# Optimization experiments

Measured on AMD Instinct MI355X. Metric: run time of the kernel, lower is better.

Reference implementation:

```python
import math
import jax, jax.numpy as jnp
import numpy as np

B, S, HID = 2, 2048, 3072
NH, HD = 32, 96            # num_heads, head_dim; num_kv_heads == num_heads (n_rep = 1)
OP = NH * HD + 2 * (NH * HD)  # 9216


def _rope_tables(seq_len, head_dim, theta=10000.0):
    inv_freq = 1.0 / (theta ** (np.arange(0, head_dim, 2, dtype=np.float32) / head_dim))
    t = np.arange(seq_len, dtype=np.float32)
    freqs = np.outer(t, inv_freq)                      # [S, HD/2]
    emb = np.concatenate([freqs, freqs], axis=-1)      # [S, HD]
    return jnp.asarray(np.cos(emb)), jnp.asarray(np.sin(emb))


def setup_inputs() -> dict:
    key = jax.random.key(0)
    k1, k2, k3 = jax.random.split(key, 3)
    hidden_states = jax.random.normal(k1, (B, S, HID), dtype=jnp.float32)
    cos, sin = _rope_tables(S, HD)
    # additive causal mask [B, 1, S, S]
    neg = jnp.finfo(jnp.float32).min
    causal = jnp.where(jnp.tril(jnp.ones((S, S), dtype=bool)), 0.0, neg)
    attention_mask = jnp.broadcast_to(causal[None, None], (B, 1, S, S)).astype(jnp.float32)
    Wqkv = jax.random.normal(k2, (HID, OP), dtype=jnp.float32) * (HID ** -0.5)
    Wo = jax.random.normal(k3, (NH * HD, HID), dtype=jnp.float32) * ((NH * HD) ** -0.5)
    return {"hidden_states": hidden_states, "cos": cos, "sin": sin,
            "attention_mask": attention_mask, "Wqkv": Wqkv, "Wo": Wo}


def _rotate_half(x):
    x1, x2 = jnp.split(x, 2, axis=-1)
    return jnp.concatenate([-x2, x1], axis=-1)


def reference(hidden_states, cos, sin, attention_mask, Wqkv, Wo):
    bsz, q_len, _ = hidden_states.shape
    qkv = hidden_states @ Wqkv                                    # [B,S,OP]
    q, k, v = jnp.split(qkv, [NH * HD, 2 * NH * HD], axis=-1)
    # [B,S,H*D] -> [B,H,S,D]
    to_bhsd = lambda t: t.reshape(bsz, q_len, NH, HD).transpose(0, 2, 1, 3)
    q, k, v = to_bhsd(q), to_bhsd(k), to_bhsd(v)
    c = cos[None, None]                                           # [1,1,S,D]
    s = sin[None, None]
    q = q * c + _rotate_half(q) * s
    k = k * c + _rotate_half(k) * s
    # num_key_value_groups == 1, so repeat_kv is identity.
    scores = jnp.einsum('bhqd,bhkd->bhqk', q, k) / math.sqrt(HD)  # [B,H,S,S]
    scores = scores + attention_mask
    attn = jax.nn.softmax(scores.astype(jnp.float32), axis=-1).astype(v.dtype)
    # dropout p=0.0 / eval -> identity
    out = jnp.einsum('bhqk,bhkd->bhqd', attn, v)                  # [B,H,S,D]
    out = out.transpose(0, 2, 1, 3).reshape(bsz, q_len, NH * HD)
    return out @ Wo                                               # [B,S,HID]
```

## Files before the change

kernel.cpp:

```cpp
#include <hip/hip_runtime.h>

typedef __bf16  bf16x8 __attribute__((ext_vector_type(8)));
typedef float   f32x4  __attribute__((ext_vector_type(4)));
typedef float   f32x16 __attribute__((ext_vector_type(16)));
typedef short   i16x8  __attribute__((ext_vector_type(8)));
typedef unsigned short u16x4 __attribute__((ext_vector_type(4)));
typedef unsigned int   u32x4 __attribute__((ext_vector_type(4)));

__device__ __forceinline__ float bf2f(unsigned short u) {
    union { unsigned int i; float f; } v; v.i = ((unsigned int)u) << 16; return v.f;
}
__device__ __forceinline__ unsigned short f2bf(float f) {
    union { float f; unsigned int i; } v; v.f = f;
    unsigned int r = v.i + 0x7FFFu + ((v.i >> 16) & 1u);
    return (unsigned short)(r >> 16);
}
__device__ __forceinline__ unsigned packbf(float lo, float hi) {
    return (unsigned)f2bf(lo) | ((unsigned)f2bf(hi) << 16);
}
__device__ __forceinline__ void gload_lds16(const void* g, void* l) {
    __builtin_amdgcn_global_load_lds(
        (const __attribute__((address_space(1))) void*)g,
        (__attribute__((address_space(3))) void*)l, 16, 0, 0);
}
__device__ __forceinline__ void pswap(unsigned &x, unsigned &y) {
#if __has_builtin(__builtin_amdgcn_permlane32_swap)
    auto r = __builtin_amdgcn_permlane32_swap((int)x, (int)y, false, false);
    x = (unsigned)r[0]; y = (unsigned)r[1];
#else
    unsigned nx = (threadIdx.x & 32) ? (unsigned)__shfl_xor((int)y, 32) : x;
    unsigned ny = (threadIdx.x & 32) ? y : (unsigned)__shfl_xor((int)x, 32);
    x = nx; y = ny;
#endif
}
__device__ __forceinline__ float partner_f(float v, int hi) {
    unsigned x = __builtin_bit_cast(unsigned, v), y = x;
    pswap(x, y);
    return __builtin_bit_cast(float, hi ? x : y);
}

__global__ __launch_bounds__(256) void cast_f32_bf16(
    const float* __restrict__ in, unsigned short* __restrict__ out, int n8)
{
    int i = blockIdx.x * 256 + threadIdx.x;
    if (i >= n8) return;
    const f32x4* p = (const f32x4*)(in + (long)i * 8);
    f32x4 a = p[0], b = p[1];
    i16x8 o;
    o[0]=(short)f2bf(a[0]); o[1]=(short)f2bf(a[1]); o[2]=(short)f2bf(a[2]); o[3]=(short)f2bf(a[3]);
    o[4]=(short)f2bf(b[0]); o[5]=(short)f2bf(b[1]); o[6]=(short)f2bf(b[2]); o[7]=(short)f2bf(b[3]);
    *(i16x8*)(out + (long)i * 8) = o;
}

__global__ __launch_bounds__(256) void transpose_cast(
    const float* __restrict__ in, unsigned short* __restrict__ out, int R, int C)
{
    __shared__ float tile[64][65];
    int c0 = blockIdx.x * 64, r0 = blockIdx.y * 64;
    int tx = threadIdx.x & 63, ty = threadIdx.x >> 6;
#pragma unroll
    for (int i = 0; i < 64; i += 4)
        tile[ty + i][tx] = in[(long)(r0 + ty + i) * C + c0 + tx];
    __syncthreads();
#pragma unroll
    for (int i = 0; i < 64; i += 4)
        out[(long)(c0 + ty + i) * R + r0 + tx] = f2bf(tile[tx][ty + i]);
}

template <int MODE>
__global__ __launch_bounds__(256) void gemm_bt(
    const unsigned short* __restrict__ A, const unsigned short* __restrict__ B,
    int K, int N,
    unsigned short* __restrict__ Qo, unsigned short* __restrict__ Ko,
    unsigned short* __restrict__ Vo, float* __restrict__ Cf)
{
    __shared__ unsigned short Al[128 * 64];
    __shared__ unsigned short Bl[128 * 64];
    const int t = threadIdx.x;
    const int w = t >> 6, l = t & 63, lhi = l >> 4, llo = l & 15;
    const int m0 = blockIdx.x * 128, n0 = blockIdx.y * 128;
    const int wmo = (w >> 1) << 6, wno = (w & 1) << 6;

    const unsigned short* ag[4];
    const unsigned short* bg[4];
#pragma unroll
    for (int i = 0; i < 4; ++i) {
        int j = i * 256 + t;
        int row = j >> 3;
        int c = (j & 7) ^ (row & 7);
        ag[i] = A + (long)(m0 + row) * K + c * 8;
        bg[i] = B + (long)(n0 + row) * K + c * 8;
    }

    f32x4 acc[4][4] = {};
    const int nkt = K >> 6;
    for (int kt = 0; kt < nkt; ++kt) {
        __syncthreads();
#pragma unroll
        for (int i = 0; i < 4; ++i) {
            gload_lds16(ag[i] + kt * 64, &Al[(i * 256 + (w << 6)) * 8]);
            gload_lds16(bg[i] + kt * 64, &Bl[(i * 256 + (w << 6)) * 8]);
        }
        __syncthreads();
#pragma unroll
        for (int kf = 0; kf < 2; ++kf) {
            bf16x8 af[4], bfv[4];
#pragma unroll
            for (int mi = 0; mi < 4; ++mi) {
                int row = wmo + mi * 16 + llo;
                int cc = (kf * 4 + lhi) ^ (row & 7);
                af[mi] = __builtin_bit_cast(bf16x8, *(const i16x8*)&Al[row * 64 + cc * 8]);
            }
#pragma unroll
            for (int ni = 0; ni < 4; ++ni) {
                int row = wno + ni * 16 + llo;
                int cc = (kf * 4 + lhi) ^ (row & 7);
                bfv[ni] = __builtin_bit_cast(bf16x8, *(const i16x8*)&Bl[row * 64 + cc * 8]);
            }
#pragma unroll
            for (int mi = 0; mi < 4; ++mi)
#pragma unroll
                for (int ni = 0; ni < 4; ++ni)
                    acc[mi][ni] = __builtin_amdgcn_mfma_f32_16x16x32_bf16(
                        af[mi], bfv[ni], acc[mi][ni], 0, 0, 0);
        }
    }

#pragma unroll
    for (int mi = 0; mi < 4; ++mi) {
        int s0g = m0 + wmo + mi * 16 + (lhi << 2);
#pragma unroll
        for (int ni = 0; ni < 4; ++ni) {
            int gcol = n0 + wno + ni * 16 + llo;
            if (MODE == 1) {
#pragma unroll
                for (int r = 0; r < 4; ++r)
                    Cf[(long)(s0g + r) * N + gcol] = acc[mi][ni][r];
            } else {
                int seg = gcol / 3072;
                int cc2 = gcol - seg * 3072;
                int h = cc2 / 96, d = cc2 - h * 96;
                int b = s0g >> 11, s = s0g & 2047;
                long bh = (long)((b << 5) + h);
                if (seg == 2) {
                    u16x4 pv;
#pragma unroll
                    for (int r = 0; r < 4; ++r) pv[r] = f2bf(acc[mi][ni][r]);
                    *(u16x4*)(Vo + (bh * 96 + d) * 2048 + s) = pv;
                } else {
                    unsigned short* dst = seg ? Ko : Qo;
#pragma unroll
                    for (int r = 0; r < 4; ++r)
                        dst[(bh * 2048 + s + r) * 96 + d] = f2bf(acc[mi][ni][r]);
                }
            }
        }
    }
}

__global__ __launch_bounds__(256) void rope_kernel(
    unsigned short* __restrict__ Qb, unsigned short* __restrict__ Kb,
    const float* __restrict__ cosT, const float* __restrict__ sinT)
{
    int i = blockIdx.x * 256 + threadIdx.x;
    int d6 = i % 6;
    int sbh = i / 6;
    int s = sbh & 2047;
    long base = (long)sbh * 96 + d6 * 8;
    const f32x4* cp = (const f32x4*)(cosT + s * 96 + d6 * 8);
    const f32x4* sp = (const f32x4*)(sinT + s * 96 + d6 * 8);
    f32x4 c0 = cp[0], c1 = cp[1], s0 = sp[0], s1 = sp[1];
    float cv[8] = {c0[0],c0[1],c0[2],c0[3],c1[0],c1[1],c1[2],c1[3]};
    float sv[8] = {s0[0],s0[1],s0[2],s0[3],s1[0],s1[1],s1[2],s1[3]};
    i16x8 qlo = *(i16x8*)(Qb + base), qhi = *(i16x8*)(Qb + base + 48);
    i16x8 klo = *(i16x8*)(Kb + base), khi = *(i16x8*)(Kb + base + 48);
    i16x8 qlo2, qhi2, klo2, khi2;
#pragma unroll
    for (int j = 0; j < 8; ++j) {
        float ql = bf2f((unsigned short)qlo[j]), qh = bf2f((unsigned short)qhi[j]);
        float kl = bf2f((unsigned short)klo[j]), kh = bf2f((unsigned short)khi[j]);
        qlo2[j] = (short)f2bf(ql * cv[j] - qh * sv[j]);
        qhi2[j] = (short)f2bf(qh * cv[j] + ql * sv[j]);
        klo2[j] = (short)f2bf(kl * cv[j] - kh * sv[j]);
        khi2[j] = (short)f2bf(kh * cv[j] + kl * sv[j]);
    }
    *(i16x8*)(Qb + base) = qlo2; *(i16x8*)(Qb + base + 48) = qhi2;
    *(i16x8*)(Kb + base) = klo2; *(i16x8*)(Kb + base + 48) = khi2;
}

__global__ __launch_bounds__(256, 2) void attn_fwd(
    const unsigned short* __restrict__ Q, const unsigned short* __restrict__ Kt,
    const unsigned short* __restrict__ Vg, unsigned short* __restrict__ O)
{
    __shared__ __align__(16) unsigned short Kl[2][64 * 128];
    __shared__ __align__(16) unsigned short Vl[2][96 * 64];
    const int t = threadIdx.x;
    const int w = t >> 6, l = t & 63;
    const int l31 = l & 31, hi = l >> 5, l7 = l & 7;
    const int bh = blockIdx.x;
    constexpr float C2 = 0.14724450f;

    const unsigned short* Kg  = Kt + (long)bh * 2048 * 96;
    const unsigned short* Vgb = Vg + (long)bh * 96 * 2048;

#define STAGE_KV(buf, tile)                                                        \
    {                                                                              \
        _Pragma("unroll")                                                          \
        for (int i_ = 0; i_ < 4; ++i_) {                                           \
            int row_ = (w << 4) + (i_ << 2) + (l >> 4);                            \
            gload_lds16(Kg + ((long)(tile) * 64 + row_) * 96 +                     \
                            (((l & 15) ^ (row_ & 7)) << 3),                        \
                        &Kl[buf][((w << 4) + (i_ << 2)) << 7]);                    \
        }                                                                          \
        _Pragma("unroll")                                                          \
        for (int i_ = 0; i_ < 3; ++i_) {                                           \
            int row_ = w * 24 + (i_ << 3) + (l >> 3);                              \
            gload_lds16(Vgb + (long)row_ * 2048 + (tile) * 64 +                    \
                            ((l7 ^ (row_ & 7)) << 3),                              \
                        &Vl[buf][(w * 24 + (i_ << 3)) << 6]);                      \
        }                                                                          \
    }

    const int b = bh >> 5, h = bh & 31;

    for (int pass = 0; pass < 2; ++pass) {
        const int qt = pass ? 15 - (int)blockIdx.y : (int)blockIdx.y;
        const int q0b = qt << 7;
        const int nkv = 2 * qt + 2;
        const int kd  = 2 * qt + (w >> 1);

        bf16x8 qf[6];
        {
            const unsigned short* qp =
                Q + ((long)bh * 2048 + q0b + (w << 5) + l31) * 96 + (hi << 3);
#pragma unroll
            for (int ks = 0; ks < 6; ++ks)
                qf[ks] = __builtin_bit_cast(bf16x8, *(const i16x8*)(qp + ks * 16));
        }

        f32x16 oa[3] = {};
        float m_r = -1e30f, l_r = 0.f;

        STAGE_KV(0, 0);
        STAGE_KV(1, 1);

        for (int kt = 0; kt < nkv; ++kt) {
            const int cb = kt & 1;
            if (kt < nkv - 1) asm volatile("s_waitcnt vmcnt(7)" ::: "memory");
            else              asm volatile("s_waitcnt vmcnt(0)" ::: "memory");
            __builtin_amdgcn_s_barrier();

            if (kt <= kd) {
                f32x16 s0 = {}, s1 = {};
                __builtin_amdgcn_s_setprio(1);
#pragma unroll
                for (int ks = 0; ks < 6; ++ks) {
                    bf16x8 k0 = __builtin_bit_cast(bf16x8, *(const i16x8*)
                        &Kl[cb][(l31 << 7) + ((((ks << 1) + hi) ^ l7) << 3)]);
                    bf16x8 k1 = __builtin_bit_cast(bf16x8, *(const i16x8*)
                        &Kl[cb][((32 + l31) << 7) + ((((ks << 1) + hi) ^ l7) << 3)]);
                    s0 = __builtin_amdgcn_mfma_f32_32x32x16_bf16(k0, qf[ks], s0, 0, 0, 0);
                    s1 = __builtin_amdgcn_mfma_f32_32x32x16_bf16(k1, qf[ks], s1, 0, 0, 0);
                }
                __builtin_amdgcn_s_setprio(0);

                if (kt == kd) {
#pragma unroll
                    for (int r = 0; r < 16; ++r) {
                        int kvl = (r & 3) + ((r >> 2) << 3) + (hi << 2);
                        if (w & 1) {
                            if (kvl > l31) s1[r] = -1e30f;
                        } else {
                            if (kvl > l31) s0[r] = -1e30f;
                            s1[r] = -1e30f;
                        }
                    }
                }
                float px = s0[0];
#pragma unroll
                for (int r = 1; r < 16; ++r) px = fmaxf(px, s0[r]);
#pragma unroll
                for (int r = 0; r < 16; ++r) px = fmaxf(px, s1[r]);
                px = fmaxf(px, partner_f(px, hi));
                if (__any(px > m_r + 54.0f)) {
                    float mnew = fmaxf(m_r, px);
                    float scl = exp2f((m_r - mnew) * C2);
                    l_r *= scl;
#pragma unroll
                    for (int tt = 0; tt < 3; ++tt)
#pragma unroll
                        for (int r = 0; r < 16; ++r) oa[tt][r] *= scl;
                    m_r = mnew;
                }
                const float mC = m_r * C2;
                float ls = 0.f;
#pragma unroll
                for (int r = 0; r < 16; ++r) {
                    s0[r] = exp2f(fmaf(s0[r], C2, -mC));
                    s1[r] = exp2f(fmaf(s1[r], C2, -mC));
                    ls += s0[r] + s1[r];
                }
                l_r += ls;
                bf16x8 pf[4];
#pragma unroll
                for (int s = 0; s < 4; ++s) {
                    const f32x16& pv = (s >= 2) ? s1 : s0;
                    const int bb = (s & 1) << 3;
                    unsigned d0 = packbf(pv[bb + 0], pv[bb + 1]);
                    unsigned d2 = packbf(pv[bb + 4], pv[bb + 5]);
                    pswap(d0, d2);
                    unsigned d1 = packbf(pv[bb + 2], pv[bb + 3]);
                    unsigned d3 = packbf(pv[bb + 6], pv[bb + 7]);
                    pswap(d1, d3);
                    pf[s] = __builtin_bit_cast(bf16x8, (u32x4){d0, d1, d2, d3});
                }
                __builtin_amdgcn_s_setprio(1);
#pragma unroll
                for (int s = 0; s < 4; ++s) {
#pragma unroll
                    for (int tt = 0; tt < 3; ++tt) {
                        bf16x8 vf = __builtin_bit_cast(bf16x8, *(const i16x8*)
                            &Vl[cb][((tt << 5) + l31) * 64 + ((((s << 1) + hi) ^ l7) << 3)]);
                        oa[tt] = __builtin_amdgcn_mfma_f32_32x32x16_bf16(vf, pf[s], oa[tt], 0, 0, 0);
                    }
                }
                __builtin_amdgcn_s_setprio(0);
            }

            asm volatile("s_waitcnt lgkmcnt(0)" ::: "memory");
            __builtin_amdgcn_s_barrier();
            if (kt + 2 < nkv) STAGE_KV(cb, kt + 2);
        }

        {
            float lt = l_r + partner_f(l_r, hi);
            float inv = 1.0f / lt;
            const int qg = q0b + (w << 5) + l31;
            unsigned short* ob = O + ((long)(b * 2048 + qg)) * 3072 + h * 96;
#pragma unroll
            for (int tt = 0; tt < 3; ++tt)
#pragma unroll
                for (int qd = 0; qd < 4; ++qd) {
                    u16x4 o4;
#pragma unroll
                    for (int j = 0; j < 4; ++j)
                        o4[j] = f2bf(oa[tt][(qd << 2) + j] * inv);
                    *(u16x4*)(ob + (tt << 5) + (qd << 3) + (hi << 2)) = o4;
                }
        }
    }
#undef STAGE_KV
}

extern "C" void kernel_launch(void* const* d_in, const int* in_sizes, int n_in,
                              void* d_out, int out_size, void* d_ws, size_t ws_size,
                              hipStream_t stream) {
    const float* hidden = (const float*)d_in[0];
    const float* cosT   = (const float*)d_in[1];
    const float* sinT   = (const float*)d_in[2];
    const float* Wqkv   = (const float*)d_in[4];
    const float* Wo     = (const float*)d_in[5];
    float* out = (float*)d_out;

    char* ws = (char*)d_ws;
    unsigned short* Ah  = (unsigned short*)ws;
    unsigned short* WqT = (unsigned short*)(ws + 25165824);
    unsigned short* Qb  = (unsigned short*)(ws + 25165824 + 56623104);
    unsigned short* Kb  = Qb + 12582912;
    unsigned short* Vb  = Kb + 12582912;

    cast_f32_bf16<<<6144, 256, 0, stream>>>(hidden, Ah, 1572864);
    transpose_cast<<<dim3(144, 48), 256, 0, stream>>>(Wqkv, WqT, 3072, 9216);
    gemm_bt<0><<<dim3(32, 72), 256, 0, stream>>>(Ah, WqT, 3072, 9216, Qb, Kb, Vb, nullptr);
    transpose_cast<<<dim3(48, 48), 256, 0, stream>>>(Wo, WqT, 3072, 3072);
    rope_kernel<<<3072, 256, 0, stream>>>(Qb, Kb, cosT, sinT);
    attn_fwd<<<dim3(64, 8), 256, 0, stream>>>(Qb, Kb, Vb, Ah);
    gemm_bt<1><<<dim3(32, 24), 256, 0, stream>>>(Ah, WqT, 3072, 3072,
                                                 nullptr, nullptr, nullptr, out);
}
```

Before: 515.4 us.

## Replace 128x128 GEMM with 256x256 double-buffered ping-pong pipelined GEMM

The single-buffered 128x128 tile GEMM, which synchronised every k-step, is replaced by a 256x256 tile kernel with 8 waves. It double-buffers LDS and interleaves global-to-LDS prefetch with MFMA phases, using explicit waitcnt, barriers and setprio. It also remaps block IDs to group workgroups, which should improve L2 locality. The larger tile raises data reuse per load, but it uses 128KB of LDS and lowers the workgroup count (192 for the output projection), which may underfill the CUs.

```diff
diff --git a/kernel.cpp b/kernel.cpp
--- a/kernel.cpp
+++ b/kernel.cpp
@@ -68,70 +68,129 @@
 }
 
 template <int MODE>
-__global__ __launch_bounds__(256) void gemm_bt(
+__global__ __launch_bounds__(512, 2) void gemm256(
     const unsigned short* __restrict__ A, const unsigned short* __restrict__ B,
-    int K, int N,
+    int K, int N, int nbx,
     unsigned short* __restrict__ Qo, unsigned short* __restrict__ Ko,
     unsigned short* __restrict__ Vo, float* __restrict__ Cf)
 {
-    __shared__ unsigned short Al[128 * 64];
-    __shared__ unsigned short Bl[128 * 64];
+    __shared__ __align__(16) unsigned short As[2][256 * 64];
+    __shared__ __align__(16) unsigned short Bs[2][256 * 64];
     const int t = threadIdx.x;
     const int w = t >> 6, l = t & 63, lhi = l >> 4, llo = l & 15;
-    const int m0 = blockIdx.x * 128, n0 = blockIdx.y * 128;
-    const int wmo = (w >> 1) << 6, wno = (w & 1) << 6;
-
-    const unsigned short* ag[4];
-    const unsigned short* bg[4];
+    const int wm = w >> 2, wn = w & 3;
+
+    const int nwg = gridDim.x, cpx = nwg >> 3;
+    const int wg = ((int)blockIdx.x & 7) * cpx + ((int)blockIdx.x >> 3);
+    const int bx = wg % nbx, by = wg / nbx;
+    const int m0 = bx << 8, n0 = by << 8;
+
+    const unsigned short* aG[4];
+    const unsigned short* bG[4];
+    int ldsOff[4];
 #pragma unroll
     for (int i = 0; i < 4; ++i) {
-        int j = i * 256 + t;
+        int j = i * 512 + t;
         int row = j >> 3;
         int c = (j & 7) ^ (row & 7);
-        ag[i] = A + (long)(m0 + row) * K + c * 8;
-        bg[i] = B + (long)(n0 + row) * K + c * 8;
-    }
-
-    f32x4 acc[4][4] = {};
-    const int nkt = K >> 6;
-    for (int kt = 0; kt < nkt; ++kt) {
-        __syncthreads();
-#pragma unroll
-        for (int i = 0; i < 4; ++i) {
-            gload_lds16(ag[i] + kt * 64, &Al[(i * 256 + (w << 6)) * 8]);
-            gload_lds16(bg[i] + kt * 64, &Bl[(i * 256 + (w << 6)) * 8]);
-        }
-        __syncthreads();
-#pragma unroll
-        for (int kf = 0; kf < 2; ++kf) {
-            bf16x8 af[4], bfv[4];
-#pragma unroll
-            for (int mi = 0; mi < 4; ++mi) {
-                int row = wmo + mi * 16 + llo;
-                int cc = (kf * 4 + lhi) ^ (row & 7);
-                af[mi] = __builtin_bit_cast(bf16x8, *(const i16x8*)&Al[row * 64 + cc * 8]);
-            }
-#pragma unroll
-            for (int ni = 0; ni < 4; ++ni) {
-                int row = wno + ni * 16 + llo;
-                int cc = (kf * 4 + lhi) ^ (row & 7);
-                bfv[ni] = __builtin_bit_cast(bf16x8, *(const i16x8*)&Bl[row * 64 + cc * 8]);
-            }
-#pragma unroll
-            for (int mi = 0; mi < 4; ++mi)
-#pragma unroll
-                for (int ni = 0; ni < 4; ++ni)
-                    acc[mi][ni] = __builtin_amdgcn_mfma_f32_16x16x32_bf16(
-                        af[mi], bfv[ni], acc[mi][ni], 0, 0, 0);
-        }
-    }
-
-#pragma unroll
-    for (int mi = 0; mi < 4; ++mi) {
-        int s0g = m0 + wmo + mi * 16 + (lhi << 2);
+        aG[i] = A + (long)(m0 + row) * K + c * 8;
+        bG[i] = B + (long)(n0 + row) * K + c * 8;
+        ldsOff[i] = (i * 512 + (w << 6)) * 8;
+    }
+    const int nkt = K >> 6, niter = nkt >> 1;
+
+#define SA(buf, half, kt) { gload_lds16(aG[(half)*2] + (long)(kt)*64, &As[buf][ldsOff[(half)*2]]); \
+                            gload_lds16(aG[(half)*2+1] + (long)(kt)*64, &As[buf][ldsOff[(half)*2+1]]); }
+#define SB(buf, half, kt) { gload_lds16(bG[(half)*2] + (long)(kt)*64, &Bs[buf][ldsOff[(half)*2]]); \
+                            gload_lds16(bG[(half)*2+1] + (long)(kt)*64, &Bs[buf][ldsOff[(half)*2+1]]); }
+#define RA(buf, mh) _Pragma("unroll") for (int mi = 0; mi < 4; ++mi) { \
+        int row = ((mh) << 7) + (wm << 6) + (mi << 4) + llo; \
+        _Pragma("unroll") for (int kk = 0; kk < 2; ++kk) { \
+            int cc = ((kk << 2) + lhi) ^ (row & 7); \
+            afr[mi*2+kk] = __builtin_bit_cast(bf16x8, *(const i16x8*)&As[buf][row*64 + cc*8]); } }
+#define RB(buf, nh, DST) _Pragma("unroll") for (int ni = 0; ni < 2; ++ni) { \
+        int row = ((nh) << 7) + (wn << 5) + (ni << 4) + llo; \
+        _Pragma("unroll") for (int kk = 0; kk < 2; ++kk) { \
+            int cc = ((kk << 2) + lhi) ^ (row & 7); \
+            DST[ni*2+kk] = __builtin_bit_cast(bf16x8, *(const i16x8*)&Bs[buf][row*64 + cc*8]); } }
+#define BARRIER asm volatile("s_barrier" ::: "memory")
+#define LGKM0  asm volatile("s_waitcnt lgkmcnt(0)" ::: "memory")
+#define MM(mh, nh, BFR) { __builtin_amdgcn_s_setprio(1); \
+    _Pragma("unroll") for (int kk = 0; kk < 2; ++kk) \
+    _Pragma("unroll") for (int mi = 0; mi < 4; ++mi) \
+    _Pragma("unroll") for (int ni = 0; ni < 2; ++ni) \
+        acc[((mh)<<2)+mi][((nh)<<1)+ni] = __builtin_amdgcn_mfma_f32_16x16x32_bf16( \
+            afr[mi*2+kk], BFR[ni*2+kk], acc[((mh)<<2)+mi][((nh)<<1)+ni], 0, 0, 0); \
+    __builtin_amdgcn_s_setprio(0); }
+
+    SA(0,0,0); SB(0,0,0); SA(0,1,0); SB(0,1,0);
+    SA(1,0,1); SB(1,0,1); SA(1,1,1); SB(1,1,1);
+    asm volatile("s_waitcnt vmcnt(8)" ::: "memory");
+    BARRIER;
+
+    f32x4 acc[8][4] = {};
+    bf16x8 afr[8], bfr0[4], bfr1[4];
+
+    for (int it = 0; it < niter; ++it) {
+        const int kt0 = it << 1;
+        const bool nl = (it < niter - 1);
+        RA(0, 0); RB(0, 0, bfr0);
+        asm volatile("s_waitcnt lgkmcnt(8)" ::: "memory");
+        BARRIER; LGKM0;
+        MM(0, 0, bfr0);
+        BARRIER;
+        RB(0, 1, bfr1);
+        if (nl) SA(0, 0, kt0 + 2);
+        BARRIER; LGKM0;
+        MM(0, 1, bfr1);
+        BARRIER;
+        RA(0, 1);
+        if (nl) SB(0, 0, kt0 + 2);
+        BARRIER; LGKM0;
+        MM(1, 1, bfr1);
+        BARRIER;
+        if (nl) SB(0, 1, kt0 + 2);
+        BARRIER;
+        MM(1, 0, bfr0);
+        if (nl) asm volatile("s_waitcnt vmcnt(6)" ::: "memory");
+        else    asm volatile("s_waitcnt vmcnt(0)" ::: "memory");
+        BARRIER;
+        RA(1, 0); RB(1, 0, bfr0);
+        if (nl) SA(0, 1, kt0 + 2);
+        asm volatile("s_waitcnt lgkmcnt(8)" ::: "memory");
+        BARRIER; LGKM0;
+        MM(0, 0, bfr0);
+        BARRIER;
+        RB(1, 1, bfr1);
+        if (nl) SA(1, 0, kt0 + 3);
+        BARRIER; LGKM0;
+        MM(0, 1, bfr1);
+        BARRIER;
+        RA(1, 1);
+        if (nl) SB(1, 0, kt0 + 3);
+        BARRIER; LGKM0;
+        MM(1, 1, bfr1);
+        BARRIER;
+        if (nl) { SB(1, 1, kt0 + 3); SA(1, 1, kt0 + 3); }
+        BARRIER;
+        MM(1, 0, bfr0);
+        asm volatile("s_waitcnt vmcnt(8)" ::: "memory");
+        BARRIER;
+    }
+#undef SA
+#undef SB
+#undef RA
+#undef RB
+#undef BARRIER
+#undef LGKM0
+#undef MM
+
+#pragma unroll
+    for (int mi = 0; mi < 8; ++mi) {
+        int s0g = m0 + ((mi >> 2) << 7) + (wm << 6) + ((mi & 3) << 4) + (lhi << 2);
 #pragma unroll
         for (int ni = 0; ni < 4; ++ni) {
-            int gcol = n0 + wno + ni * 16 + llo;
+            int gcol = n0 + ((ni >> 1) << 7) + (wn << 5) + ((ni & 1) << 4) + llo;
             if (MODE == 1) {
 #pragma unroll
                 for (int r = 0; r < 4; ++r)
@@ -371,10 +430,10 @@
 
     cast_f32_bf16<<<6144, 256, 0, stream>>>(hidden, Ah, 1572864);
     transpose_cast<<<dim3(144, 48), 256, 0, stream>>>(Wqkv, WqT, 3072, 9216);
-    gemm_bt<0><<<dim3(32, 72), 256, 0, stream>>>(Ah, WqT, 3072, 9216, Qb, Kb, Vb, nullptr);
+    gemm256<0><<<576, 512, 0, stream>>>(Ah, WqT, 3072, 9216, 16, Qb, Kb, Vb, nullptr);
     transpose_cast<<<dim3(48, 48), 256, 0, stream>>>(Wo, WqT, 3072, 3072);
     rope_kernel<<<3072, 256, 0, stream>>>(Qb, Kb, cosT, sinT);
     attn_fwd<<<dim3(64, 8), 256, 0, stream>>>(Qb, Kb, Vb, Ah);
-    gemm_bt<1><<<dim3(32, 24), 256, 0, stream>>>(Ah, WqT, 3072, 3072,
-                                                 nullptr, nullptr, nullptr, out);
-}
+    gemm256<1><<<192, 512, 0, stream>>>(Ah, WqT, 3072, 3072, 16,
+                                        nullptr, nullptr, nullptr, out);
+}
```

Result: no change. 508.1 us (-1.4%).
